# Optimization experiments

Hardware: AMD Instinct MI355X
Metric: run time of the kernel (lower is better)

The kernel has to match this reference:

```python
import jax, jax.numpy as jnp
import numpy as np

B, D, O, E, K = 8192, 2048, 2048, 8, 2


def setup_inputs() -> dict:
    key = jax.random.key(0)
    k1, k2, k3, k4 = jax.random.split(key, 4)
    x = jax.random.normal(k1, (B, D), dtype=jnp.float32)
    # router: Linear(D -> E)
    router_w = jax.random.normal(k2, (E, D), dtype=jnp.float32) * (1.0 / np.sqrt(D))
    router_b = jnp.zeros((E,), dtype=jnp.float32)
    # experts: [E, O, D] weight (xavier-uniform-like scale), [E, O] bias (zeros)
    lim = np.sqrt(6.0 / (D + O))
    expert_w = jax.random.uniform(k3, (E, O, D), dtype=jnp.float32, minval=-lim, maxval=lim)
    expert_b = jnp.zeros((E, O), dtype=jnp.float32)
    return {"x": x, "router_w": router_w, "router_b": router_b,
            "expert_w": expert_w, "expert_b": expert_b}


def reference(x, router_w, router_b, expert_w, expert_b):
    # router logits [B, E]
    logits = x @ router_w.T + router_b
    top_vals, top_idx = jax.lax.top_k(logits, K)          # [B, K]
    routing_weights = jax.nn.softmax(top_vals, axis=-1)   # softmax over top-k logits
    # dense per-(token, expert) combine weight [B, E]; zero for unselected experts
    onehot = jax.nn.one_hot(top_idx, E, dtype=x.dtype)    # [B, K, E]
    w_be = jnp.einsum('bk,bke->be', routing_weights, onehot)
    # per-expert linear, weighted combine (loop over small fixed E)
    out = jnp.zeros((x.shape[0], O), dtype=x.dtype)
    for e in range(E):
        out = out + w_be[:, e:e + 1] * (x @ expert_w[e].T + expert_b[e])
    return out
```

## Files before the change

### kernel.cpp

```cpp
#include <hip/hip_runtime.h>
#include <stdint.h>

#define NB 8192
#define ND 2048
#define NO 2048
#define NE 8
#define BK 64
#define NT (ND / BK)
#define BM 256
#define BN 256

typedef __bf16 bf16x8 __attribute__((ext_vector_type(8)));
typedef float floatx4 __attribute__((ext_vector_type(4)));

__device__ __forceinline__ unsigned short f2bf(float f) {
    union { float f; uint32_t u; } v; v.f = f;
    uint32_t u = v.u;
    return (unsigned short)((u + 0x7FFFu + ((u >> 16) & 1u)) >> 16);
}

__global__ __launch_bounds__(256) void cvt_zero_kernel(
        const float* __restrict__ w, unsigned short* __restrict__ ob,
        float* __restrict__ out) {
    const int n4W = NE * NO * ND / 4;
    const int n4O = NB * NO / 4;
    int i = blockIdx.x * blockDim.x + threadIdx.x;
    int stride = gridDim.x * blockDim.x;
    for (; i < n4W + n4O; i += stride) {
        if (i < n4W) {
            float4 v = ((const float4*)w)[i];
            ushort4 o;
            o.x = f2bf(v.x); o.y = f2bf(v.y); o.z = f2bf(v.z); o.w = f2bf(v.w);
            ((ushort4*)ob)[i] = o;
        } else {
            float4 z = {0.f, 0.f, 0.f, 0.f};
            ((float4*)out)[i - n4W] = z;
        }
    }
}

__global__ __launch_bounds__(256) void router_topk_kernel(const float* __restrict__ x,
        const float* __restrict__ rw, const float* __restrict__ rb,
        unsigned short* __restrict__ xbf,
        int* __restrict__ i0a, int* __restrict__ i1a,
        float* __restrict__ w0a, float* __restrict__ w1a,
        int* __restrict__ cnt) {
    if (blockIdx.x == 0 && threadIdx.x < NE) cnt[threadIdx.x] = 0;
    const int wave = threadIdx.x >> 6;
    const int lane = threadIdx.x & 63;
    const int t = blockIdx.x * 4 + wave;
    const float4* xp = (const float4*)(x + (size_t)t * ND);
    const float4* rp = (const float4*)rw;
    ushort4* xo = (ushort4*)(xbf + (size_t)t * ND);
    float acc[NE];
#pragma unroll
    for (int e = 0; e < NE; e++) acc[e] = 0.f;
#pragma unroll
    for (int i = 0; i < ND / 256; i++) {
        int idx = i * 64 + lane;
        float4 xv = xp[idx];
        ushort4 o;
        o.x = f2bf(xv.x); o.y = f2bf(xv.y); o.z = f2bf(xv.z); o.w = f2bf(xv.w);
        xo[idx] = o;
#pragma unroll
        for (int e = 0; e < NE; e++) {
            float4 rv = rp[(size_t)e * (ND / 4) + idx];
            acc[e] += xv.x * rv.x + xv.y * rv.y + xv.z * rv.z + xv.w * rv.w;
        }
    }
#pragma unroll
    for (int e = 0; e < NE; e++) {
        float v = acc[e];
#pragma unroll
        for (int s = 32; s > 0; s >>= 1) v += __shfl_xor(v, s, 64);
        acc[e] = v;
    }
    if (lane == 0) {
        float lg[NE];
#pragma unroll
        for (int e = 0; e < NE; e++) lg[e] = acc[e] + rb[e];
        int i0 = 0; float v0 = lg[0];
#pragma unroll
        for (int e = 1; e < NE; e++) if (lg[e] > v0) { v0 = lg[e]; i0 = e; }
        int i1 = -1; float v1 = -3.4e38f;
#pragma unroll
        for (int e = 0; e < NE; e++) if (e != i0 && lg[e] > v1) { v1 = lg[e]; i1 = e; }
        float ex = expf(v1 - v0);
        float inv = 1.f / (1.f + ex);
        i0a[t] = i0; i1a[t] = i1;
        w0a[t] = inv; w1a[t] = ex * inv;
    }
}

__global__ __launch_bounds__(256) void compact_kernel(
        const int* __restrict__ i0a, const int* __restrict__ i1a,
        const float* __restrict__ w0a, const float* __restrict__ w1a,
        int* __restrict__ cnt, int* __restrict__ tok, float* __restrict__ wl) {
    const int lane = threadIdx.x & 63;
    const int gw = (blockIdx.x * 256 + threadIdx.x) >> 6;
    const int t = gw * 64 + lane;
#pragma unroll
    for (int which = 0; which < 2; which++) {
        int sel   = which ? i1a[t] : i0a[t];
        float w   = which ? w1a[t] : w0a[t];
        unsigned long long m[NE];
#pragma unroll
        for (int e = 0; e < NE; e++) m[e] = __ballot(sel == e);
        int slot = __popcll(m[sel] & ((1ull << lane) - 1ull));
        int base = 0;
        if (lane < NE) base = atomicAdd(&cnt[lane], (int)__popcll(m[lane]));
        base = __shfl(base, sel, 64);
        tok[sel * NB + base + slot] = t;
        wl[sel * NB + base + slot]  = w;
    }
}

#define GLL16(g, l) __builtin_amdgcn_global_load_lds( \
    (const __attribute__((address_space(1))) void*)(g), \
    (__attribute__((address_space(3))) void*)(l), 16, 0, 0)

__global__ __launch_bounds__(512, 2) void moe_gemm_kernel(
        const unsigned short* __restrict__ xbf, const unsigned short* __restrict__ wbf,
        const float* __restrict__ eb, const int* __restrict__ cntArr,
        const int* __restrict__ listTok, const float* __restrict__ listW,
        float* __restrict__ out) {
    __shared__ unsigned short sA[2][BM * BK];
    __shared__ unsigned short sB[2][BN * BK];

    const int e = blockIdx.z, mt = blockIdx.y, nt = blockIdx.x;
    const int cnt = cntArr[e];
    if (mt * BM >= cnt) return;
    const int tid = threadIdx.x;

    const char* gA[4]; const char* gB[4];
    int ldsOff[4];
#pragma unroll
    for (int i = 0; i < 4; i++) {
        int cid = i * 512 + tid;
        int prow = cid >> 3;
        int pcol = (cid & 7) * 16;
        int scol = pcol ^ ((prow & 7) << 4);
        int gr = mt * BM + prow;
        int tk = (gr < cnt) ? listTok[e * NB + gr] : 0;
        gA[i] = (const char*)xbf + (size_t)tk * (ND * 2) + scol;
        gB[i] = (const char*)wbf + ((size_t)e * NO + (size_t)nt * BN + prow) * (ND * 2) + scol;
        ldsOff[i] = cid * 16;
    }

    const int wave = tid >> 6, lane = tid & 63;
    const int wm = (wave >> 2) * 128;
    const int wn = (wave & 3) * 64;
    const int lr = lane & 15, lq = lane >> 4;
    const int xorv = (lr & 7) << 4;
    int roA[8], roB[4];
#pragma unroll
    for (int mi = 0; mi < 8; mi++) roA[mi] = (wm + mi * 16 + lr) * (BK * 2) + ((lq * 16) ^ xorv);
#pragma unroll
    for (int nj = 0; nj < 4; nj++) roB[nj] = (wn + nj * 16 + lr) * (BK * 2) + ((lq * 16) ^ xorv);

    floatx4 acc[8][4];
#pragma unroll
    for (int mi = 0; mi < 8; mi++)
#pragma unroll
        for (int nj = 0; nj < 4; nj++) acc[mi][nj] = (floatx4){0.f, 0.f, 0.f, 0.f};

#pragma unroll
    for (int b = 0; b < 2; b++) {
#pragma unroll
        for (int i = 0; i < 4; i++) {
            GLL16(gA[i], (char*)sA[b] + ldsOff[i]);
            GLL16(gB[i], (char*)sB[b] + ldsOff[i]);
            gA[i] += 2 * BK; gB[i] += 2 * BK;
        }
    }

#pragma unroll 1
    for (int t = 0; t < NT; t++) {
        const int cur = t & 1;
        if (t + 1 < NT) { asm volatile("s_waitcnt vmcnt(8)" ::: "memory"); }
        else           { asm volatile("s_waitcnt vmcnt(0)" ::: "memory"); }
        __builtin_amdgcn_s_barrier();

        const unsigned short* sAc = sA[cur];
        const unsigned short* sBc = sB[cur];
#pragma unroll
        for (int kk = 0; kk < 2; kk++) {
            bf16x8 af[8], bfr[4];
#pragma unroll
            for (int mi = 0; mi < 8; mi++)
                af[mi] = *(const bf16x8*)((const char*)sAc + (roA[mi] ^ (kk * 64)));
#pragma unroll
            for (int nj = 0; nj < 4; nj++)
                bfr[nj] = *(const bf16x8*)((const char*)sBc + (roB[nj] ^ (kk * 64)));
            __builtin_amdgcn_s_setprio(1);
#pragma unroll
            for (int mi = 0; mi < 8; mi++)
#pragma unroll
                for (int nj = 0; nj < 4; nj++)
                    acc[mi][nj] = __builtin_amdgcn_mfma_f32_16x16x32_bf16(af[mi], bfr[nj], acc[mi][nj], 0, 0, 0);
            __builtin_amdgcn_s_setprio(0);
        }

        asm volatile("s_waitcnt lgkmcnt(0)" ::: "memory");
        __builtin_amdgcn_s_barrier();
        if (t + 2 < NT) {
#pragma unroll
            for (int i = 0; i < 4; i++) {
                GLL16(gA[i], (char*)sA[cur] + ldsOff[i]);
                GLL16(gB[i], (char*)sB[cur] + ldsOff[i]);
                gA[i] += 2 * BK; gB[i] += 2 * BK;
            }
        }
    }

    float bias[4];
#pragma unroll
    for (int nj = 0; nj < 4; nj++)
        bias[nj] = eb[(size_t)e * NO + nt * BN + wn + nj * 16 + lr];
#pragma unroll
    for (int mi = 0; mi < 8; mi++) {
#pragma unroll
        for (int r = 0; r < 4; r++) {
            int m = wm + mi * 16 + lq * 4 + r;
            int gr = mt * BM + m;
            if (gr < cnt) {
                int tk   = listTok[e * NB + gr];
                float wg = listW[e * NB + gr];
                float* op = out + (size_t)tk * NO + nt * BN + wn + lr;
#pragma unroll
                for (int nj = 0; nj < 4; nj++)
                    atomicAdd(op + nj * 16, wg * (acc[mi][nj][r] + bias[nj]));
            }
        }
    }
}

extern "C" void kernel_launch(void* const* d_in, const int* in_sizes, int n_in,
                              void* d_out, int out_size, void* d_ws, size_t ws_size,
                              hipStream_t stream) {
    const float* x        = (const float*)d_in[0];
    const float* router_w = (const float*)d_in[1];
    const float* router_b = (const float*)d_in[2];
    const float* expert_w = (const float*)d_in[3];
    const float* expert_b = (const float*)d_in[4];
    float* out = (float*)d_out;
    char* ws = (char*)d_ws;

    unsigned short* xbf = (unsigned short*)ws;
    unsigned short* wbf = (unsigned short*)(ws + 33554432);
    size_t o = 100663296;
    int*   tokL = (int*)(ws + o);   o += NE * NB * 4;
    float* wL   = (float*)(ws + o); o += NE * NB * 4;
    int*   i0a  = (int*)(ws + o);   o += NB * 4;
    int*   i1a  = (int*)(ws + o);   o += NB * 4;
    float* w0a  = (float*)(ws + o); o += NB * 4;
    float* w1a  = (float*)(ws + o); o += NB * 4;
    int*   cnt  = (int*)(ws + o);   o += 128;

    router_topk_kernel<<<NB / 4, 256, 0, stream>>>(x, router_w, router_b, xbf,
                                                   i0a, i1a, w0a, w1a, cnt);
    cvt_zero_kernel<<<2048, 256, 0, stream>>>(expert_w, wbf, out);
    compact_kernel<<<NB / 64 / 4, 256, 0, stream>>>(i0a, i1a, w0a, w1a, cnt, tokL, wL);
    moe_gemm_kernel<<<dim3(NO / BN, NB / BM, NE), 512, 0, stream>>>(
        xbf, wbf, expert_b, cnt, tokL, wL, out);
}
```

Measured before the change: 575.7 us.

## Split MoE GEMM tiles into half-tiles with an interleaved load/MFMA pipeline

Restructures the expert GEMM main loop. Each 256x256 block tile is split into four 128x128 quadrants, and LDS staging works on per-half buffers, so global-to-LDS loads for upcoming K-steps are issued between quadrant MFMA phases instead of once per K-step. Wave-to-output mapping changes to 64x32 sub-tiles in each quadrant, which cuts the fragment registers held at once. The aim is to overlap memory traffic with compute more finely, at the cost of many more barriers per iteration.

```diff
diff --git a/kernel.cpp b/kernel.cpp
--- a/kernel.cpp
+++ b/kernel.cpp
@@ -119,118 +119,159 @@
     (const __attribute__((address_space(1))) void*)(g), \
     (__attribute__((address_space(3))) void*)(l), 16, 0, 0)
 
+#define BAR __builtin_amdgcn_s_barrier()
+#define WAITL asm volatile("s_waitcnt lgkmcnt(0)" ::: "memory")
+
+#define LDA(HALFPTR) do {                                                   \
+    const char* _p = (const char*)(HALFPTR);                                \
+    _Pragma("unroll") for (int mi = 0; mi < 4; mi++)                        \
+        _Pragma("unroll") for (int kk = 0; kk < 2; kk++)                    \
+            af[mi][kk] = *(const bf16x8*)(_p + offA[mi][kk]);               \
+} while (0)
+
+#define LDB(HALFPTR) do {                                                   \
+    const char* _p = (const char*)(HALFPTR);                                \
+    _Pragma("unroll") for (int nj = 0; nj < 2; nj++)                        \
+        _Pragma("unroll") for (int kk = 0; kk < 2; kk++)                    \
+            bfr[nj][kk] = *(const bf16x8*)(_p + offB[nj][kk]);              \
+} while (0)
+
+#define MMAC(MH, NH) do {                                                   \
+    __builtin_amdgcn_s_setprio(1);                                          \
+    _Pragma("unroll") for (int kk = 0; kk < 2; kk++)                        \
+        _Pragma("unroll") for (int mi = 0; mi < 4; mi++)                    \
+            _Pragma("unroll") for (int nj = 0; nj < 2; nj++)                \
+                acc[(MH)*4+mi][(NH)*2+nj] =                                 \
+                    __builtin_amdgcn_mfma_f32_16x16x32_bf16(                \
+                        af[mi][kk], bfr[nj][kk],                            \
+                        acc[(MH)*4+mi][(NH)*2+nj], 0, 0, 0);                \
+    __builtin_amdgcn_s_setprio(0);                                          \
+} while (0)
+
+#define STG_A(D, H, KT) do { if ((KT) < NT) {                               \
+    GLL16(bA[H][0] + (size_t)(KT) * 128, (char*)sA[D][H] + tid * 16);       \
+    GLL16(bA[H][1] + (size_t)(KT) * 128, (char*)sA[D][H] + 8192 + tid * 16);\
+} } while (0)
+#define STG_B(D, H, KT) do { if ((KT) < NT) {                               \
+    GLL16(bB[H][0] + (size_t)(KT) * 128, (char*)sB[D][H] + tid * 16);       \
+    GLL16(bB[H][1] + (size_t)(KT) * 128, (char*)sB[D][H] + 8192 + tid * 16);\
+} } while (0)
+
 __global__ __launch_bounds__(512, 2) void moe_gemm_kernel(
         const unsigned short* __restrict__ xbf, const unsigned short* __restrict__ wbf,
         const float* __restrict__ eb, const int* __restrict__ cntArr,
         const int* __restrict__ listTok, const float* __restrict__ listW,
         float* __restrict__ out) {
-    __shared__ unsigned short sA[2][BM * BK];
-    __shared__ unsigned short sB[2][BN * BK];
+    __shared__ unsigned short sA[2][2][128 * 64];
+    __shared__ unsigned short sB[2][2][128 * 64];
 
     const int e = blockIdx.z, mt = blockIdx.y, nt = blockIdx.x;
     const int cnt = cntArr[e];
     if (mt * BM >= cnt) return;
     const int tid = threadIdx.x;
 
-    const char* gA[4]; const char* gB[4];
-    int ldsOff[4];
-#pragma unroll
-    for (int i = 0; i < 4; i++) {
-        int cid = i * 512 + tid;
-        int prow = cid >> 3;
-        int pcol = (cid & 7) * 16;
-        int scol = pcol ^ ((prow & 7) << 4);
-        int gr = mt * BM + prow;
-        int tk = (gr < cnt) ? listTok[e * NB + gr] : 0;
-        gA[i] = (const char*)xbf + (size_t)tk * (ND * 2) + scol;
-        gB[i] = (const char*)wbf + ((size_t)e * NO + (size_t)nt * BN + prow) * (ND * 2) + scol;
-        ldsOff[i] = cid * 16;
+    const int prow0 = tid >> 3;
+    const int prow1 = 64 + (tid >> 3);
+    const int scol  = ((tid & 7) * 16) ^ (((tid >> 3) & 7) << 4);
+    const char* bA[2][2]; const char* bB[2][2];
+#pragma unroll
+    for (int h = 0; h < 2; h++) {
+        int g0 = mt * BM + h * 128 + prow0;
+        int g1 = mt * BM + h * 128 + prow1;
+        int tk0 = (g0 < cnt) ? listTok[e * NB + g0] : 0;
+        int tk1 = (g1 < cnt) ? listTok[e * NB + g1] : 0;
+        bA[h][0] = (const char*)xbf + (size_t)tk0 * (ND * 2) + scol;
+        bA[h][1] = (const char*)xbf + (size_t)tk1 * (ND * 2) + scol;
+        bB[h][0] = (const char*)wbf + ((size_t)e * NO + (size_t)nt * BN + h * 128 + prow0) * (ND * 2) + scol;
+        bB[h][1] = (const char*)wbf + ((size_t)e * NO + (size_t)nt * BN + h * 128 + prow1) * (ND * 2) + scol;
     }
 
     const int wave = tid >> 6, lane = tid & 63;
-    const int wm = (wave >> 2) * 128;
-    const int wn = (wave & 3) * 64;
+    const int wm2 = wave >> 2;
+    const int wn2 = wave & 3;
     const int lr = lane & 15, lq = lane >> 4;
     const int xorv = (lr & 7) << 4;
-    int roA[8], roB[4];
-#pragma unroll
-    for (int mi = 0; mi < 8; mi++) roA[mi] = (wm + mi * 16 + lr) * (BK * 2) + ((lq * 16) ^ xorv);
-#pragma unroll
-    for (int nj = 0; nj < 4; nj++) roB[nj] = (wn + nj * 16 + lr) * (BK * 2) + ((lq * 16) ^ xorv);
-
+    int offA[4][2], offB[2][2];
+#pragma unroll
+    for (int mi = 0; mi < 4; mi++)
+#pragma unroll
+        for (int kk = 0; kk < 2; kk++)
+            offA[mi][kk] = (wm2 * 64 + mi * 16 + lr) * 128 + ((kk * 64 + lq * 16) ^ xorv);
+#pragma unroll
+    for (int nj = 0; nj < 2; nj++)
+#pragma unroll
+        for (int kk = 0; kk < 2; kk++)
+            offB[nj][kk] = (wn2 * 32 + nj * 16 + lr) * 128 + ((kk * 64 + lq * 16) ^ xorv);
+
+    bf16x8 af[4][2], bfr[2][2];
     floatx4 acc[8][4];
 #pragma unroll
-    for (int mi = 0; mi < 8; mi++)
-#pragma unroll
-        for (int nj = 0; nj < 4; nj++) acc[mi][nj] = (floatx4){0.f, 0.f, 0.f, 0.f};
-
-#pragma unroll
-    for (int b = 0; b < 2; b++) {
-#pragma unroll
-        for (int i = 0; i < 4; i++) {
-            GLL16(gA[i], (char*)sA[b] + ldsOff[i]);
-            GLL16(gB[i], (char*)sB[b] + ldsOff[i]);
-            gA[i] += 2 * BK; gB[i] += 2 * BK;
-        }
-    }
+    for (int i = 0; i < 8; i++)
+#pragma unroll
+        for (int j = 0; j < 4; j++) acc[i][j] = (floatx4){0.f, 0.f, 0.f, 0.f};
+
+    STG_A(0, 0, 0); STG_B(0, 1, 0); STG_A(0, 1, 0); STG_B(0, 0, 0);
+    STG_A(1, 0, 1); STG_B(1, 1, 1);
+    asm volatile("s_waitcnt vmcnt(4)" ::: "memory");
+    BAR;
 
 #pragma unroll 1
-    for (int t = 0; t < NT; t++) {
-        const int cur = t & 1;
-        if (t + 1 < NT) { asm volatile("s_waitcnt vmcnt(8)" ::: "memory"); }
-        else           { asm volatile("s_waitcnt vmcnt(0)" ::: "memory"); }
-        __builtin_amdgcn_s_barrier();
-
-        const unsigned short* sAc = sA[cur];
-        const unsigned short* sBc = sB[cur];
-#pragma unroll
-        for (int kk = 0; kk < 2; kk++) {
-            bf16x8 af[8], bfr[4];
-#pragma unroll
-            for (int mi = 0; mi < 8; mi++)
-                af[mi] = *(const bf16x8*)((const char*)sAc + (roA[mi] ^ (kk * 64)));
-#pragma unroll
-            for (int nj = 0; nj < 4; nj++)
-                bfr[nj] = *(const bf16x8*)((const char*)sBc + (roB[nj] ^ (kk * 64)));
-            __builtin_amdgcn_s_setprio(1);
-#pragma unroll
-            for (int mi = 0; mi < 8; mi++)
-#pragma unroll
-                for (int nj = 0; nj < 4; nj++)
-                    acc[mi][nj] = __builtin_amdgcn_mfma_f32_16x16x32_bf16(af[mi], bfr[nj], acc[mi][nj], 0, 0, 0);
-            __builtin_amdgcn_s_setprio(0);
-        }
-
-        asm volatile("s_waitcnt lgkmcnt(0)" ::: "memory");
-        __builtin_amdgcn_s_barrier();
-        if (t + 2 < NT) {
-#pragma unroll
-            for (int i = 0; i < 4; i++) {
-                GLL16(gA[i], (char*)sA[cur] + ldsOff[i]);
-                GLL16(gB[i], (char*)sB[cur] + ldsOff[i]);
-                gA[i] += 2 * BK; gB[i] += 2 * BK;
-            }
-        }
-    }
-
-    float bias[4];
-#pragma unroll
-    for (int nj = 0; nj < 4; nj++)
-        bias[nj] = eb[(size_t)e * NO + nt * BN + wn + nj * 16 + lr];
-#pragma unroll
-    for (int mi = 0; mi < 8; mi++) {
-#pragma unroll
-        for (int r = 0; r < 4; r++) {
-            int m = wm + mi * 16 + lq * 4 + r;
-            int gr = mt * BM + m;
-            if (gr < cnt) {
-                int tk   = listTok[e * NB + gr];
-                float wg = listW[e * NB + gr];
-                float* op = out + (size_t)tk * NO + nt * BN + wn + lr;
-#pragma unroll
-                for (int nj = 0; nj < 4; nj++)
-                    atomicAdd(op + nj * 16, wg * (acc[mi][nj][r] + bias[nj]));
-            }
+    for (int i = 0; i < NT / 2; i++) {
+        const int t1 = 2 * i + 1, t2 = 2 * i + 2, t3 = 2 * i + 3;
+        LDA(sA[0][0]); LDB(sB[0][0]);
+        STG_A(1, 1, t1);
+        BAR; MMAC(0, 0); WAITL; BAR;
+        LDB(sB[0][1]);
+        STG_B(1, 0, t1);
+        BAR; MMAC(0, 1); WAITL; BAR;
+        LDA(sA[0][1]);
+        STG_A(0, 0, t2);
+        BAR; MMAC(1, 1); WAITL; BAR;
+        LDB(sB[0][0]);
+        STG_B(0, 1, t2);
+        BAR; MMAC(1, 0); WAITL;
+        if (t2 < NT) { asm volatile("s_waitcnt vmcnt(4)" ::: "memory"); }
+        else         { asm volatile("s_waitcnt vmcnt(0)" ::: "memory"); }
+        BAR;
+        LDA(sA[1][0]); LDB(sB[1][0]);
+        STG_A(0, 1, t2);
+        BAR; MMAC(0, 0); WAITL; BAR;
+        LDB(sB[1][1]);
+        STG_B(0, 0, t2);
+        BAR; MMAC(0, 1); WAITL; BAR;
+        LDA(sA[1][1]);
+        STG_A(1, 0, t3);
+        BAR; MMAC(1, 1); WAITL; BAR;
+        LDB(sB[1][0]);
+        STG_B(1, 1, t3);
+        BAR; MMAC(1, 0); WAITL;
+        asm volatile("s_waitcnt vmcnt(4)" ::: "memory");
+        BAR;
+    }
+
+    float ebv[4];
+#pragma unroll
+    for (int nh = 0; nh < 2; nh++)
+#pragma unroll
+        for (int nj = 0; nj < 2; nj++)
+            ebv[nh * 2 + nj] = eb[(size_t)e * NO + nt * BN + nh * 128 + wn2 * 32 + nj * 16 + lr];
+#pragma unroll
+    for (int mh = 0; mh < 2; mh++)
+#pragma unroll
+    for (int mi = 0; mi < 4; mi++)
+#pragma unroll
+    for (int r = 0; r < 4; r++) {
+        int gr = mt * BM + mh * 128 + wm2 * 64 + mi * 16 + lq * 4 + r;
+        if (gr < cnt) {
+            int tk   = listTok[e * NB + gr];
+            float wg = listW[e * NB + gr];
+            float* op = out + (size_t)tk * NO + nt * BN + lr;
+#pragma unroll
+            for (int nh = 0; nh < 2; nh++)
+#pragma unroll
+            for (int nj = 0; nj < 2; nj++)
+                atomicAdd(op + nh * 128 + wn2 * 32 + nj * 16,
+                          wg * (acc[mh * 4 + mi][nh * 2 + nj][r] + ebv[nh * 2 + nj]));
         }
     }
 }
```

Measured after the change: 557.5 us. 1.03x faster.
